# Kernel tuning notes

Hardware: AMD Instinct MI355X
Metric: run time of the kernel (lower is better)

The kernel has to match this reference:

```python
import jax, jax.numpy as jnp
import numpy as np

N_NODES = 100000
N_EDGES = 1600000
D = 128


def setup_inputs() -> dict:
    key = jax.random.key(0)
    ks = jax.random.split(key, 10)
    s = 1.0 / np.sqrt(D)
    return {
        "feat": jax.random.normal(ks[0], (N_NODES, D), dtype=jnp.float32),
        "W_self0": jax.random.normal(ks[1], (D, D), dtype=jnp.float32) * s,
        "W_neigh0": jax.random.normal(ks[2], (D, D), dtype=jnp.float32) * s,
        "b0": jnp.zeros((D,), dtype=jnp.float32),
        "W_self1": jax.random.normal(ks[3], (D, D), dtype=jnp.float32) * s,
        "W_neigh1": jax.random.normal(ks[4], (D, D), dtype=jnp.float32) * s,
        "b1": jnp.zeros((D,), dtype=jnp.float32),
        "ln_g": jnp.ones((D,), dtype=jnp.float32),
        "ln_b": jnp.zeros((D,), dtype=jnp.float32),
        "edge_src": jax.random.randint(ks[5], (N_EDGES,), 0, N_NODES, dtype=jnp.int32),
        "edge_dst": jax.random.randint(ks[6], (N_EDGES,), 0, N_NODES, dtype=jnp.int32),
        "in_deg": jax.random.randint(ks[7], (N_NODES,), 1, 64, dtype=jnp.int32),
    }


def _sage_layer(h, src, dst, inv_deg, W_self, W_neigh, b):
    # mean aggregation over incoming neighbors: gather -> segment_sum -> scale
    msg = jax.ops.segment_sum(h[src], dst, num_segments=N_NODES)  # [N, d]
    h_neigh = msg * inv_deg[:, None]
    return h @ W_self + h_neigh @ W_neigh + b


def _layer_norm(x, g, b, eps=1e-5):
    mu = jnp.mean(x, axis=-1, keepdims=True)
    var = jnp.mean((x - mu) ** 2, axis=-1, keepdims=True)
    return (x - mu) * jax.lax.rsqrt(var + eps) * g + b


def reference(feat, W_self0, W_neigh0, b0, W_self1, W_neigh1, b1, ln_g, ln_b,
              edge_src, edge_dst, in_deg):
    # Eval mode: dropout = identity, no EmbeddingSelector / reg loss.
    inv_deg = 1.0 / jnp.maximum(in_deg, 1).astype(feat.dtype)
    h = _sage_layer(feat, edge_src, edge_dst, inv_deg, W_self0, W_neigh0, b0)
    h = _layer_norm(h, ln_g, ln_b)
    h = jax.nn.relu(h)
    h = _sage_layer(h, edge_src, edge_dst, inv_deg, W_self1, W_neigh1, b1)
    return h
```

## Files before the change

### kernel.cpp

```cpp
#include <hip/hip_runtime.h>

#define D 128
#define NN 100000
#define PB 391
#define EPB 4096
#define PREP_BLKS 12756

typedef __attribute__((ext_vector_type(8))) short short8;
typedef __attribute__((ext_vector_type(16))) float floatx16;
typedef __attribute__((ext_vector_type(2))) float floatx2;

__device__ inline unsigned short bf16_rne(float f) {
    unsigned int u = __float_as_uint(f);
    u += 0x7fff + ((u >> 16) & 1);
    return (unsigned short)(u >> 16);
}
__device__ inline unsigned char fp8_enc1(float f) {
    return (unsigned char)(__builtin_amdgcn_cvt_pk_fp8_f32(f, f, 0, false) & 0xff);
}

__global__ __launch_bounds__(256) void prep_count_kernel(
    const float* __restrict__ feat, unsigned short* __restrict__ feat16,
    unsigned char* __restrict__ feat8,
    const float* __restrict__ Ws0, const float* __restrict__ Wn0,
    const float* __restrict__ Ws1, const float* __restrict__ Wn1,
    unsigned short* __restrict__ wt0, unsigned short* __restrict__ wt1,
    const int* __restrict__ dst, unsigned int* __restrict__ bucketCnt,
    unsigned int* __restrict__ blockBase, int E)
{
    __shared__ unsigned int h[PB];
    int bid = blockIdx.x;
    if (bid < 12500) {
        int i = bid * 256 + threadIdx.x;
        float4 v = *(const float4*)(feat + (size_t)i * 4);
        unsigned short u[4] = { bf16_rne(v.x), bf16_rne(v.y), bf16_rne(v.z), bf16_rne(v.w) };
        *(uint2*)(feat16 + (size_t)i * 4) = *(uint2*)u;
        int w = __builtin_amdgcn_cvt_pk_fp8_f32(v.x, v.y, 0, false);
        w = __builtin_amdgcn_cvt_pk_fp8_f32(v.z, v.w, w, true);
        ((unsigned int*)feat8)[i] = (unsigned int)w;
    } else if (bid < PREP_BLKS) {
        int i = (bid - 12500) * 256 + threadIdx.x;
        int layer = i >> 15;
        int r = i & 32767;
        int n = r >> 8;
        int k = r & 255;
        const float* Ws = layer ? Ws1 : Ws0;
        const float* Wn = layer ? Wn1 : Wn0;
        float v = (k < 128) ? Ws[(size_t)k * 128 + n] : Wn[(size_t)(k - 128) * 128 + n];
        unsigned short* wt = layer ? wt1 : wt0;
        wt[(size_t)n * 256 + k] = bf16_rne(v);
    } else {
        const int b = bid - PREP_BLKS;
        const int t = threadIdx.x;
        for (int i = t; i < PB; i += 256) h[i] = 0;
        __syncthreads();
        const int base = b * EPB;
#pragma unroll
        for (int k = 0; k < EPB / 256; k++) {
            int e = base + k * 256 + t;
            if (e < E) atomicAdd(&h[(unsigned)dst[e] >> 8], 1u);
        }
        __syncthreads();
        for (int i = t; i < PB; i += 256) {
            unsigned int c = h[i];
            unsigned int o = 0;
            if (c) o = atomicAdd(&bucketCnt[i], c);
            blockBase[(size_t)b * PB + i] = o;
        }
    }
}

__global__ __launch_bounds__(512) void part_scan_kernel(
    const unsigned int* __restrict__ bucketCnt, unsigned int* __restrict__ bucketStart,
    int E)
{
    __shared__ unsigned int sd[512];
    int t = threadIdx.x;
    unsigned int v = (t < PB) ? bucketCnt[t] : 0u;
    sd[t] = v; __syncthreads();
    for (int off = 1; off < 512; off <<= 1) {
        unsigned int x = (t >= off) ? sd[t - off] : 0u;
        __syncthreads();
        sd[t] += x;
        __syncthreads();
    }
    if (t < PB) bucketStart[t] = sd[t] - v;
    if (t == 0) bucketStart[PB] = (unsigned int)E;
}

__global__ __launch_bounds__(256) void part_scatter_kernel(
    const int* __restrict__ src, const int* __restrict__ dst,
    const unsigned int* __restrict__ bucketStart,
    const unsigned int* __restrict__ blockBase,
    unsigned int* __restrict__ pairs, int E)
{
    __shared__ unsigned int h[PB];
    const int t = threadIdx.x;
    const int b = blockIdx.x;
    for (int i = t; i < PB; i += 256) h[i] = 0;
    __syncthreads();
    const int base = b * EPB;
#pragma unroll
    for (int k = 0; k < EPB / 256; k++) {
        int e = base + k * 256 + t;
        if (e < E) {
            unsigned int d = (unsigned int)dst[e];
            unsigned int bk = d >> 8;
            unsigned int lr = atomicAdd(&h[bk], 1u);
            unsigned int pos = bucketStart[bk] + blockBase[(size_t)b * PB + bk] + lr;
            pairs[pos] = ((unsigned int)src[e] << 8) | (d & 255u);
        }
    }
}

__global__ __launch_bounds__(256) void part_fine_kernel(
    const unsigned int* __restrict__ pairs, const unsigned int* __restrict__ bucketStart,
    int* __restrict__ row_ptr, int* __restrict__ col, int N, int E)
{
    __shared__ unsigned int h[256], sc[256], pos[256];
    const int t = threadIdx.x;
    const int b = blockIdx.x;
    h[t] = 0;
    __syncthreads();
    const unsigned int ebeg = bucketStart[b];
    const unsigned int eend = bucketStart[b + 1];
    for (unsigned int i = ebeg + t; i < eend; i += 256)
        atomicAdd(&h[pairs[i] & 255u], 1u);
    __syncthreads();
    sc[t] = h[t]; __syncthreads();
    for (int off = 1; off < 256; off <<= 1) {
        unsigned int x = (t >= off) ? sc[t - off] : 0u;
        __syncthreads();
        sc[t] += x;
        __syncthreads();
    }
    unsigned int excl = sc[t] - h[t];
    int node = b * 256 + t;
    if (node < N) row_ptr[node] = (int)(ebeg + excl);
    pos[t] = ebeg + excl;
    if (b == 0 && t == 0) row_ptr[N] = E;
    __syncthreads();
    for (unsigned int i = ebeg + t; i < eend; i += 256) {
        unsigned int p = pairs[i];
        unsigned int w = atomicAdd(&pos[p & 255u], 1u);
        col[w] = (int)(p >> 8);
    }
}

__global__ __launch_bounds__(256) void gather8_kernel(
    const unsigned char* __restrict__ h8, const int* __restrict__ row_ptr,
    const int* __restrict__ col, const int* __restrict__ in_deg,
    unsigned short* __restrict__ msg16, int N)
{
    const int wave = threadIdx.x >> 6;
    const int lane = threadIdx.x & 63;
    const int quad = lane >> 4;
    const int ln16 = lane & 15;
    const int node = (blockIdx.x * 4 + wave) * 4 + quad;
    if (node >= N) return;

    const size_t lo = (size_t)ln16 * 8;
    int beg = row_ptr[node];
    int end = row_ptr[node + 1];

    float f[8] = {0.f,0.f,0.f,0.f,0.f,0.f,0.f,0.f};
    int j = beg;
    for (; j + 4 <= end; j += 4) {
        int c0 = col[j], c1 = col[j + 1], c2 = col[j + 2], c3 = col[j + 3];
        uint2 u0 = *(const uint2*)(h8 + (size_t)c0 * D + lo);
        uint2 u1 = *(const uint2*)(h8 + (size_t)c1 * D + lo);
        uint2 u2 = *(const uint2*)(h8 + (size_t)c2 * D + lo);
        uint2 u3 = *(const uint2*)(h8 + (size_t)c3 * D + lo);
#pragma unroll
        for (int q = 0; q < 4; q++) {
            uint2 u = q == 0 ? u0 : q == 1 ? u1 : q == 2 ? u2 : u3;
            floatx2 p0 = __builtin_amdgcn_cvt_pk_f32_fp8((int)u.x, false);
            floatx2 p1 = __builtin_amdgcn_cvt_pk_f32_fp8((int)u.x, true);
            floatx2 p2 = __builtin_amdgcn_cvt_pk_f32_fp8((int)u.y, false);
            floatx2 p3 = __builtin_amdgcn_cvt_pk_f32_fp8((int)u.y, true);
            f[0] += p0.x; f[1] += p0.y; f[2] += p1.x; f[3] += p1.y;
            f[4] += p2.x; f[5] += p2.y; f[6] += p3.x; f[7] += p3.y;
        }
    }
    for (; j < end; ++j) {
        uint2 u = *(const uint2*)(h8 + (size_t)col[j] * D + lo);
        floatx2 p0 = __builtin_amdgcn_cvt_pk_f32_fp8((int)u.x, false);
        floatx2 p1 = __builtin_amdgcn_cvt_pk_f32_fp8((int)u.x, true);
        floatx2 p2 = __builtin_amdgcn_cvt_pk_f32_fp8((int)u.y, false);
        floatx2 p3 = __builtin_amdgcn_cvt_pk_f32_fp8((int)u.y, true);
        f[0] += p0.x; f[1] += p0.y; f[2] += p1.x; f[3] += p1.y;
        f[4] += p2.x; f[5] += p2.y; f[6] += p3.x; f[7] += p3.y;
    }
    int dg = in_deg[node];
    float invd = 1.f / (float)(dg > 1 ? dg : 1);
    unsigned short us[8];
#pragma unroll
    for (int i = 0; i < 8; i++) us[i] = bf16_rne(f[i] * invd);
    *(uint4*)(msg16 + (size_t)node * D + ln16 * 8) = *(const uint4*)us;
}

__global__ __launch_bounds__(256) void mfma32_kernel(
    const unsigned short* __restrict__ A16, const unsigned short* __restrict__ Msg16,
    const unsigned short* __restrict__ Wt,
    const float* __restrict__ bias,
    const float* __restrict__ ln_g, const float* __restrict__ ln_b,
    unsigned short* __restrict__ Out16, unsigned char* __restrict__ Out8,
    float* __restrict__ Out32, int N, int do_ln)
{
    __shared__ unsigned short sB[32768];

    const int tid  = threadIdx.x;
    const int wave = tid >> 6;
    const int lane = tid & 63;
    const int half = lane >> 5;
    const int n32  = lane & 31;
    const int brow0 = blockIdx.x * 128;
    const int wrow0 = brow0 + wave * 32;

#pragma unroll
    for (int i = 0; i < 16; i++) {
        int idx = tid + i * 256;
        int n = idx & 127;
        int c = idx >> 7;
        uint4 w = *(const uint4*)(Wt + (size_t)n * 256 + c * 8);
        int hs = c >> 4, kc = (c >> 1) & 7, hf = c & 1;
        int ct = n >> 5, nn = n & 31;
        int chunk = (((ct * 2 + hs) * 8 + kc) * 2 + hf) * 32 + nn;
        *(uint4*)&sB[(size_t)chunk * 8] = w;
    }
    __syncthreads();

    const int arow = wrow0 + n32;
    const bool arv = arow < N;
    const size_t koff = (size_t)half * 8;

    floatx16 acc[4];
#pragma unroll
    for (int ct = 0; ct < 4; ct++)
#pragma unroll
        for (int r = 0; r < 16; r++) acc[ct][r] = 0.f;

#pragma unroll
    for (int hs = 0; hs < 2; hs++) {
        const unsigned short* Asrc = hs ? Msg16 : A16;
#pragma unroll
        for (int kc = 0; kc < 8; kc++) {
            short8 a;
            if (arv) a = *(const short8*)(Asrc + (size_t)arow * D + kc * 16 + koff);
            else     a = (short8){0,0,0,0,0,0,0,0};
#pragma unroll
            for (int ct = 0; ct < 4; ct++) {
                short8 b = *(const short8*)&sB[((size_t)((ct * 2 + hs) * 8 + kc) * 64 + lane) * 8];
                acc[ct] = __builtin_amdgcn_mfma_f32_32x32x16_bf16(a, b, acc[ct], 0, 0, 0);
            }
        }
    }

    float bb[4];
#pragma unroll
    for (int ct = 0; ct < 4; ct++) bb[ct] = bias[ct * 32 + n32];

    float v[4][16];
#pragma unroll
    for (int ct = 0; ct < 4; ct++)
#pragma unroll
        for (int r = 0; r < 16; r++) v[ct][r] = acc[ct][r] + bb[ct];

    __syncthreads();

    if (do_ln) {
        float gg[4], be[4];
#pragma unroll
        for (int ct = 0; ct < 4; ct++) {
            gg[ct] = ln_g[ct * 32 + n32];
            be[ct] = ln_b[ct * 32 + n32];
        }
        float s[16], s2[16];
#pragma unroll
        for (int r = 0; r < 16; r++) {
            s[r]  = v[0][r] + v[1][r] + v[2][r] + v[3][r];
            s2[r] = v[0][r]*v[0][r] + v[1][r]*v[1][r] + v[2][r]*v[2][r] + v[3][r]*v[3][r];
        }
#pragma unroll
        for (int off = 1; off < 32; off <<= 1) {
#pragma unroll
            for (int r = 0; r < 16; r++) {
                s[r]  += __shfl_xor(s[r],  off);
                s2[r] += __shfl_xor(s2[r], off);
            }
        }
        unsigned short* sO16 = sB;
        unsigned char*  sO8  = (unsigned char*)sB + 32768;
#pragma unroll
        for (int r = 0; r < 16; r++) {
            float mean = s[r] * (1.f / 128.f);
            float var  = s2[r] * (1.f / 128.f) - mean * mean;
            float rstd = rsqrtf(var + 1e-5f);
            int brow = wave * 32 + (r & 3) + 8 * (r >> 2) + 4 * half;
#pragma unroll
            for (int ct = 0; ct < 4; ct++) {
                float t = (v[ct][r] - mean) * rstd * gg[ct] + be[ct];
                t = t > 0.f ? t : 0.f;
                sO16[brow * 128 + ct * 32 + n32] = bf16_rne(t);
                sO8 [brow * 128 + ct * 32 + n32] = fp8_enc1(t);
            }
        }
        __syncthreads();
#pragma unroll
        for (int i = 0; i < 8; i++) {
            int ch = tid + i * 256;
            if (brow0 + (ch >> 4) < N)
                *(uint4*)(Out16 + (size_t)brow0 * D + ch * 8) = *(const uint4*)&sO16[ch * 8];
        }
#pragma unroll
        for (int i = 0; i < 4; i++) {
            int ch = tid + i * 256;
            if (brow0 + (ch >> 3) < N)
                *(uint4*)(Out8 + (size_t)brow0 * D + ch * 16) = *(const uint4*)&sO8[ch * 16];
        }
    } else {
        float* sO32 = (float*)sB;
#pragma unroll
        for (int r = 0; r < 16; r++) {
            int brow = wave * 32 + (r & 3) + 8 * (r >> 2) + 4 * half;
#pragma unroll
            for (int ct = 0; ct < 4; ct++)
                sO32[brow * 128 + ct * 32 + n32] = v[ct][r];
        }
        __syncthreads();
#pragma unroll
        for (int i = 0; i < 16; i++) {
            int ch = tid + i * 256;
            if (brow0 + (ch >> 5) < N)
                *(uint4*)(Out32 + (size_t)brow0 * D + ch * 4) = *(const uint4*)&sO32[ch * 4];
        }
    }
}

extern "C" void kernel_launch(void* const* d_in, const int* in_sizes, int n_in,
                              void* d_out, int out_size, void* d_ws, size_t ws_size,
                              hipStream_t stream)
{
    const float* feat = (const float*)d_in[0];
    const float* Ws0  = (const float*)d_in[1];
    const float* Wn0  = (const float*)d_in[2];
    const float* b0   = (const float*)d_in[3];
    const float* Ws1  = (const float*)d_in[4];
    const float* Wn1  = (const float*)d_in[5];
    const float* b1   = (const float*)d_in[6];
    const float* lng  = (const float*)d_in[7];
    const float* lnb  = (const float*)d_in[8];
    const int* esrc   = (const int*)d_in[9];
    const int* edst   = (const int*)d_in[10];
    const int* indeg  = (const int*)d_in[11];

    const int N = NN;
    const int E = in_sizes[9];

    float* out = (float*)d_out;

    const int nblk = (E + EPB - 1) / EPB;
    char* ws = (char*)d_ws;
    size_t o = 0;
    auto alloc = [&](size_t bytes) { char* p = ws + o; o += (bytes + 15) & ~(size_t)15; return p; };
    unsigned short* feat16 = (unsigned short*)alloc((size_t)N * D * 2);
    int* col     = (int*)alloc((size_t)E * 4);
    int* row_ptr = (int*)alloc((size_t)(N + 1) * 4);
    unsigned short* wt0 = (unsigned short*)alloc(128 * 256 * 2);
    unsigned short* wt1 = (unsigned short*)alloc(128 * 256 * 2);
    size_t csr_bytes = (size_t)(512 + 512 + (size_t)nblk * PB + E) * 4 + 64;
    char* regD = alloc((size_t)N * D * 2 > csr_bytes ? (size_t)N * D * 2 : csr_bytes);
    unsigned int* bucketCnt   = (unsigned int*)regD;
    unsigned int* bucketStart = bucketCnt + 512;
    unsigned int* blockBase   = bucketStart + 512;
    unsigned int* pairs       = blockBase + (size_t)nblk * PB;
    unsigned short* h116 = (unsigned short*)regD;

    unsigned short* msg0  = (unsigned short*)d_out;
    unsigned char*  feat8 = (unsigned char*)d_out + (size_t)N * D * 2;
    unsigned char*  h18   = (unsigned char*)d_out + (size_t)N * D * 3;
    unsigned short* msg1  = feat16;
    (void)ws_size;

    const int gemm_blocks = (N + 127) / 128;
    const int gather_blocks = (N + 15) / 16;

    hipMemsetAsync(bucketCnt, 0, 512 * 4, stream);
    prep_count_kernel<<<PREP_BLKS + nblk, 256, 0, stream>>>(
        feat, feat16, feat8, Ws0, Wn0, Ws1, Wn1, wt0, wt1,
        edst, bucketCnt, blockBase, E);

    part_scan_kernel<<<1, 512, 0, stream>>>(bucketCnt, bucketStart, E);
    part_scatter_kernel<<<nblk, 256, 0, stream>>>(esrc, edst, bucketStart, blockBase, pairs, E);
    part_fine_kernel<<<PB, 256, 0, stream>>>(pairs, bucketStart, row_ptr, col, N, E);

    gather8_kernel<<<gather_blocks, 256, 0, stream>>>(feat8, row_ptr, col, indeg, msg0, N);
    mfma32_kernel<<<gemm_blocks, 256, 0, stream>>>(
        feat16, msg0, wt0, b0, lng, lnb, h116, h18, nullptr, N, 1);

    gather8_kernel<<<gather_blocks, 256, 0, stream>>>(h18, row_ptr, col, indeg, msg1, N);
    mfma32_kernel<<<gemm_blocks, 256, 0, stream>>>(
        h116, msg1, wt1, b1, nullptr, nullptr, nullptr, nullptr, out, N, 0);
}
```

Measured before the change: 317.3 us.

## Pre-swizzle weights into MFMA fragment layout and drop LDS staging in GEMM

The prep kernel now writes the transposed bf16 weights directly in the per-lane MFMA fragment order, so the GEMM kernel reads B fragments straight from global memory (L2/L1 cached) instead of staging 64KB into shared memory. The LDS-based output staging is also removed; results are stored directly from accumulators with scalar per-element writes, and launch bounds request 4 blocks per SM. This removes LDS use and block barriers to raise occupancy, at the cost of uncoalesced 2-byte, 1-byte and 4-byte global stores and repeated global B-fragment loads.

Result: slower. 345.2 us (+8.8%).

```diff
diff --git a/kernel.cpp b/kernel.cpp
--- a/kernel.cpp
+++ b/kernel.cpp
@@ -48,7 +48,11 @@
         const float* Wn = layer ? Wn1 : Wn0;
         float v = (k < 128) ? Ws[(size_t)k * 128 + n] : Wn[(size_t)(k - 128) * 128 + n];
         unsigned short* wt = layer ? wt1 : wt0;
-        wt[(size_t)n * 256 + k] = bf16_rne(v);
+        int ct = n >> 5, nn = n & 31;
+        int hs = k >> 7, k7 = k & 127;
+        int kc = k7 >> 4, hf = (k7 >> 3) & 1, j = k7 & 7;
+        int frag = ((((ct * 2 + hs) * 8 + kc) * 2 + hf) * 32 + nn) * 8 + j;
+        wt[frag] = bf16_rne(v);
     } else {
         const int b = bid - PREP_BLKS;
         const int t = threadIdx.x;
@@ -199,7 +203,7 @@
     *(uint4*)(msg16 + (size_t)node * D + ln16 * 8) = *(const uint4*)us;
 }
 
-__global__ __launch_bounds__(256) void mfma32_kernel(
+__global__ __launch_bounds__(256, 4) void mfma32_kernel(
     const unsigned short* __restrict__ A16, const unsigned short* __restrict__ Msg16,
     const unsigned short* __restrict__ Wt,
     const float* __restrict__ bias,
@@ -207,8 +211,6 @@
     unsigned short* __restrict__ Out16, unsigned char* __restrict__ Out8,
     float* __restrict__ Out32, int N, int do_ln)
 {
-    __shared__ unsigned short sB[32768];
-
     const int tid  = threadIdx.x;
     const int wave = tid >> 6;
     const int lane = tid & 63;
@@ -217,19 +219,6 @@
     const int brow0 = blockIdx.x * 128;
     const int wrow0 = brow0 + wave * 32;
 
-#pragma unroll
-    for (int i = 0; i < 16; i++) {
-        int idx = tid + i * 256;
-        int n = idx & 127;
-        int c = idx >> 7;
-        uint4 w = *(const uint4*)(Wt + (size_t)n * 256 + c * 8);
-        int hs = c >> 4, kc = (c >> 1) & 7, hf = c & 1;
-        int ct = n >> 5, nn = n & 31;
-        int chunk = (((ct * 2 + hs) * 8 + kc) * 2 + hf) * 32 + nn;
-        *(uint4*)&sB[(size_t)chunk * 8] = w;
-    }
-    __syncthreads();
-
     const int arow = wrow0 + n32;
     const bool arv = arow < N;
     const size_t koff = (size_t)half * 8;
@@ -250,23 +239,18 @@
             else     a = (short8){0,0,0,0,0,0,0,0};
 #pragma unroll
             for (int ct = 0; ct < 4; ct++) {
-                short8 b = *(const short8*)&sB[((size_t)((ct * 2 + hs) * 8 + kc) * 64 + lane) * 8];
+                short8 b = *(const short8*)(Wt + ((size_t)((ct * 2 + hs) * 8 + kc) * 64 + lane) * 8);
                 acc[ct] = __builtin_amdgcn_mfma_f32_32x32x16_bf16(a, b, acc[ct], 0, 0, 0);
             }
         }
     }
 
-    float bb[4];
-#pragma unroll
-    for (int ct = 0; ct < 4; ct++) bb[ct] = bias[ct * 32 + n32];
-
-    float v[4][16];
-#pragma unroll
-    for (int ct = 0; ct < 4; ct++)
-#pragma unroll
-        for (int r = 0; r < 16; r++) v[ct][r] = acc[ct][r] + bb[ct];
-
-    __syncthreads();
+#pragma unroll
+    for (int ct = 0; ct < 4; ct++) {
+        float bb = bias[ct * 32 + n32];
+#pragma unroll
+        for (int r = 0; r < 16; r++) acc[ct][r] += bb;
+    }
 
     if (do_ln) {
         float gg[4], be[4];
@@ -278,8 +262,9 @@
         float s[16], s2[16];
 #pragma unroll
         for (int r = 0; r < 16; r++) {
-            s[r]  = v[0][r] + v[1][r] + v[2][r] + v[3][r];
-            s2[r] = v[0][r]*v[0][r] + v[1][r]*v[1][r] + v[2][r]*v[2][r] + v[3][r]*v[3][r];
+            s[r]  = acc[0][r] + acc[1][r] + acc[2][r] + acc[3][r];
+            s2[r] = acc[0][r]*acc[0][r] + acc[1][r]*acc[1][r]
+                  + acc[2][r]*acc[2][r] + acc[3][r]*acc[3][r];
         }
 #pragma unroll
         for (int off = 1; off < 32; off <<= 1) {
@@ -289,50 +274,31 @@
                 s2[r] += __shfl_xor(s2[r], off);
             }
         }
-        unsigned short* sO16 = sB;
-        unsigned char*  sO8  = (unsigned char*)sB + 32768;
 #pragma unroll
         for (int r = 0; r < 16; r++) {
             float mean = s[r] * (1.f / 128.f);
             float var  = s2[r] * (1.f / 128.f) - mean * mean;
             float rstd = rsqrtf(var + 1e-5f);
-            int brow = wave * 32 + (r & 3) + 8 * (r >> 2) + 4 * half;
-#pragma unroll
-            for (int ct = 0; ct < 4; ct++) {
-                float t = (v[ct][r] - mean) * rstd * gg[ct] + be[ct];
-                t = t > 0.f ? t : 0.f;
-                sO16[brow * 128 + ct * 32 + n32] = bf16_rne(t);
-                sO8 [brow * 128 + ct * 32 + n32] = fp8_enc1(t);
+            int row = wrow0 + (r & 3) + 8 * (r >> 2) + 4 * half;
+            if (row < N) {
+#pragma unroll
+                for (int ct = 0; ct < 4; ct++) {
+                    float t = (acc[ct][r] - mean) * rstd * gg[ct] + be[ct];
+                    t = t > 0.f ? t : 0.f;
+                    Out16[(size_t)row * D + ct * 32 + n32] = bf16_rne(t);
+                    Out8 [(size_t)row * D + ct * 32 + n32] = fp8_enc1(t);
+                }
             }
         }
-        __syncthreads();
-#pragma unroll
-        for (int i = 0; i < 8; i++) {
-            int ch = tid + i * 256;
-            if (brow0 + (ch >> 4) < N)
-                *(uint4*)(Out16 + (size_t)brow0 * D + ch * 8) = *(const uint4*)&sO16[ch * 8];
-        }
-#pragma unroll
-        for (int i = 0; i < 4; i++) {
-            int ch = tid + i * 256;
-            if (brow0 + (ch >> 3) < N)
-                *(uint4*)(Out8 + (size_t)brow0 * D + ch * 16) = *(const uint4*)&sO8[ch * 16];
-        }
     } else {
-        float* sO32 = (float*)sB;
 #pragma unroll
         for (int r = 0; r < 16; r++) {
-            int brow = wave * 32 + (r & 3) + 8 * (r >> 2) + 4 * half;
-#pragma unroll
-            for (int ct = 0; ct < 4; ct++)
-                sO32[brow * 128 + ct * 32 + n32] = v[ct][r];
-        }
-        __syncthreads();
-#pragma unroll
-        for (int i = 0; i < 16; i++) {
-            int ch = tid + i * 256;
-            if (brow0 + (ch >> 5) < N)
-                *(uint4*)(Out32 + (size_t)brow0 * D + ch * 4) = *(const uint4*)&sO32[ch * 4];
+            int row = wrow0 + (r & 3) + 8 * (r >> 2) + 4 * half;
+            if (row < N) {
+#pragma unroll
+                for (int ct = 0; ct < 4; ct++)
+                    Out32[(size_t)row * D + ct * 32 + n32] = acc[ct][r];
+            }
         }
     }
 }
```

## Stage A tiles via async global-to-LDS loads, pre-swizzle weights in prep

Applied to the files above, without the earlier changes.

The prep kernel now writes the bf16 weights directly in MFMA fragment order, so the GEMM kernel reads B fragments straight from global memory instead of first staging them into LDS. The A operands (self features and aggregated messages) are loaded asynchronously into swizzled LDS using global_load_lds, and split waitcnt barriers let the self-half MFMAs begin while the message half is still in flight. Launch bounds request two blocks per CU. The cost is that B fragments now come from global/L2 on every block, and correctness depends on the hand-written vmcnt counts and the XOR swizzle lining up.

New measurement: 322.7 us. About the same (+1.7%).

```diff
diff --git a/kernel.cpp b/kernel.cpp
--- a/kernel.cpp
+++ b/kernel.cpp
@@ -17,6 +17,12 @@
 }
 __device__ inline unsigned char fp8_enc1(float f) {
     return (unsigned char)(__builtin_amdgcn_cvt_pk_fp8_f32(f, f, 0, false) & 0xff);
+}
+
+__device__ inline void gload_lds16(const void* g, void* l) {
+    __builtin_amdgcn_global_load_lds(
+        (const __attribute__((address_space(1))) unsigned int*)g,
+        (__attribute__((address_space(3))) unsigned int*)l, 16, 0, 0);
 }
 
 __global__ __launch_bounds__(256) void prep_count_kernel(
@@ -48,7 +54,11 @@
         const float* Wn = layer ? Wn1 : Wn0;
         float v = (k < 128) ? Ws[(size_t)k * 128 + n] : Wn[(size_t)(k - 128) * 128 + n];
         unsigned short* wt = layer ? wt1 : wt0;
-        wt[(size_t)n * 256 + k] = bf16_rne(v);
+        int ct = n >> 5, nn = n & 31;
+        int hs = k >> 7, k7 = k & 127;
+        int kc = k7 >> 4, hf = (k7 >> 3) & 1, j = k7 & 7;
+        int frag = ((((ct * 2 + hs) * 8 + kc) * 2 + hf) * 32 + nn) * 8 + j;
+        wt[frag] = bf16_rne(v);
     } else {
         const int b = bid - PREP_BLKS;
         const int t = threadIdx.x;
@@ -199,7 +209,7 @@
     *(uint4*)(msg16 + (size_t)node * D + ln16 * 8) = *(const uint4*)us;
 }
 
-__global__ __launch_bounds__(256) void mfma32_kernel(
+__global__ __launch_bounds__(256, 2) void mfma32_kernel(
     const unsigned short* __restrict__ A16, const unsigned short* __restrict__ Msg16,
     const unsigned short* __restrict__ Wt,
     const float* __restrict__ bias,
@@ -207,7 +217,7 @@
     unsigned short* __restrict__ Out16, unsigned char* __restrict__ Out8,
     float* __restrict__ Out32, int N, int do_ln)
 {
-    __shared__ unsigned short sB[32768];
+    __shared__ char smem[65536];
 
     const int tid  = threadIdx.x;
     const int wave = tid >> 6;
@@ -217,22 +227,26 @@
     const int brow0 = blockIdx.x * 128;
     const int wrow0 = brow0 + wave * 32;
 
-#pragma unroll
-    for (int i = 0; i < 16; i++) {
-        int idx = tid + i * 256;
-        int n = idx & 127;
-        int c = idx >> 7;
-        uint4 w = *(const uint4*)(Wt + (size_t)n * 256 + c * 8);
-        int hs = c >> 4, kc = (c >> 1) & 7, hf = c & 1;
-        int ct = n >> 5, nn = n & 31;
-        int chunk = (((ct * 2 + hs) * 8 + kc) * 2 + hf) * 32 + nn;
-        *(uint4*)&sB[(size_t)chunk * 8] = w;
-    }
-    __syncthreads();
-
-    const int arow = wrow0 + n32;
-    const bool arv = arow < N;
-    const size_t koff = (size_t)half * 8;
+    {
+        const char* gA = (const char*)(A16 + (size_t)brow0 * D);
+        const char* gM = (const char*)(Msg16 + (size_t)brow0 * D);
+        const int R16 = (N - brow0) * 16;
+        char* ldst = smem + wave * 1024;
+#pragma unroll
+        for (int i = 0; i < 8; i++) {
+            int K = i * 256 + tid;
+            int swz = K ^ ((K >> 4) & 15);
+            size_t gb = (size_t)(K < R16 ? swz : 0) * 16;
+            gload_lds16(gA + gb, ldst + i * 4096);
+        }
+#pragma unroll
+        for (int i = 0; i < 8; i++) {
+            int K = i * 256 + tid;
+            int swz = K ^ ((K >> 4) & 15);
+            size_t gb = (size_t)(K < R16 ? swz : 0) * 16;
+            gload_lds16(gM + gb, ldst + 32768 + i * 4096);
+        }
+    }
 
     floatx16 acc[4];
 #pragma unroll
@@ -240,19 +254,36 @@
 #pragma unroll
         for (int r = 0; r < 16; r++) acc[ct][r] = 0.f;
 
-#pragma unroll
-    for (int hs = 0; hs < 2; hs++) {
-        const unsigned short* Asrc = hs ? Msg16 : A16;
-#pragma unroll
-        for (int kc = 0; kc < 8; kc++) {
-            short8 a;
-            if (arv) a = *(const short8*)(Asrc + (size_t)arow * D + kc * 16 + koff);
-            else     a = (short8){0,0,0,0,0,0,0,0};
-#pragma unroll
-            for (int ct = 0; ct < 4; ct++) {
-                short8 b = *(const short8*)&sB[((size_t)((ct * 2 + hs) * 8 + kc) * 64 + lane) * 8];
-                acc[ct] = __builtin_amdgcn_mfma_f32_32x32x16_bf16(a, b, acc[ct], 0, 0, 0);
-            }
+    const int rowb = (wave * 32 + n32) * 256;
+    const int xr   = n32 & 15;
+
+    asm volatile("s_waitcnt vmcnt(8)" ::: "memory");
+    __builtin_amdgcn_s_barrier();
+    asm volatile("" ::: "memory");
+
+#pragma unroll
+    for (int kc = 0; kc < 8; kc++) {
+        int c = (kc * 2 + half) ^ xr;
+        short8 a = *(const short8*)(smem + rowb + c * 16);
+#pragma unroll
+        for (int ct = 0; ct < 4; ct++) {
+            short8 b = *(const short8*)(Wt + ((size_t)((ct * 2 + 0) * 8 + kc) * 64 + lane) * 8);
+            acc[ct] = __builtin_amdgcn_mfma_f32_32x32x16_bf16(a, b, acc[ct], 0, 0, 0);
+        }
+    }
+
+    asm volatile("s_waitcnt vmcnt(0)" ::: "memory");
+    __builtin_amdgcn_s_barrier();
+    asm volatile("" ::: "memory");
+
+#pragma unroll
+    for (int kc = 0; kc < 8; kc++) {
+        int c = (kc * 2 + half) ^ xr;
+        short8 a = *(const short8*)(smem + 32768 + rowb + c * 16);
+#pragma unroll
+        for (int ct = 0; ct < 4; ct++) {
+            short8 b = *(const short8*)(Wt + ((size_t)((ct * 2 + 1) * 8 + kc) * 64 + lane) * 8);
+            acc[ct] = __builtin_amdgcn_mfma_f32_32x32x16_bf16(a, b, acc[ct], 0, 0, 0);
         }
     }
 
@@ -289,8 +320,8 @@
                 s2[r] += __shfl_xor(s2[r], off);
             }
         }
-        unsigned short* sO16 = sB;
-        unsigned char*  sO8  = (unsigned char*)sB + 32768;
+        unsigned short* sO16 = (unsigned short*)smem;
+        unsigned char*  sO8  = (unsigned char*)smem + 32768;
 #pragma unroll
         for (int r = 0; r < 16; r++) {
             float mean = s[r] * (1.f / 128.f);
@@ -319,7 +350,7 @@
                 *(uint4*)(Out8 + (size_t)brow0 * D + ch * 16) = *(const uint4*)&sO8[ch * 16];
         }
     } else {
-        float* sO32 = (float*)sB;
+        float* sO32 = (float*)smem;
 #pragma unroll
         for (int r = 0; r < 16; r++) {
             int brow = wave * 32 + (r & 3) + 8 * (r >> 2) + 4 * half;
```
